# Kernel tuning notes

Hardware: AMD Instinct MI355X
Metric: run time of the kernel (lower is better)

Reference implementation:

```python
import jax, jax.numpy as jnp
import numpy as np

DEPTH = 15  # complete binary tree, N = 2**DEPTH - 1 nodes, heap layout


def setup_inputs() -> dict:
    key = jax.random.key(0)
    ks = jax.random.split(key, 9)
    D, H = 512, 512
    N = 2 ** DEPTH - 1
    s = 0.02
    return {
        "x": jax.random.normal(ks[0], (N, D), jnp.float32),
        "Wi": jax.random.normal(ks[1], (H, D + H), jnp.float32) * s,
        "bi": jax.random.normal(ks[2], (H,), jnp.float32) * s,
        "Wf": jax.random.normal(ks[3], (H, D + H), jnp.float32) * s,
        "bf": jax.random.normal(ks[4], (H,), jnp.float32) * s,
        "Wo": jax.random.normal(ks[5], (H, D + H), jnp.float32) * s,
        "bo": jax.random.normal(ks[6], (H,), jnp.float32) * s,
        "Wu": jax.random.normal(ks[7], (H, D + H), jnp.float32) * s,
        "bu": jax.random.normal(ks[8], (H,), jnp.float32) * s,
    }


def _tree_lstm(x, Wi, bi, Wf, bf, Wo, bo, Wu, bu):
    # Child-Sum Tree-LSTM on a complete binary tree in heap layout.
    # Levels processed bottom-up; each level is fully batched.
    N, D = x.shape
    H = Wi.shape[0]
    sig, tanh = jax.nn.sigmoid, jnp.tanh
    h = jnp.zeros((N, H), x.dtype)
    c = jnp.zeros((N, H), x.dtype)
    for lvl in range(DEPTH - 1, -1, -1):
        start = 2 ** lvl - 1
        cnt = 2 ** lvl
        xl = x[start:start + cnt]  # [cnt, D]
        if lvl == DEPTH - 1:
            # leaf_forward: h_children = 0, no forget gates
            xh = jnp.concatenate([xl, jnp.zeros((cnt, H), x.dtype)], axis=1)
            i = sig(xh @ Wi.T + bi)
            o = sig(xh @ Wo.T + bo)
            u = tanh(xh @ Wu.T + bu)
            cl = i * u
        else:
            cs = 2 * start + 1  # first child index of this level
            ch = h[cs:cs + 2 * cnt].reshape(cnt, 2, H)
            cc = c[cs:cs + 2 * cnt].reshape(cnt, 2, H)
            h_l, h_r = ch[:, 0], ch[:, 1]
            hsum = h_l + h_r  # child-sum
            xh = jnp.concatenate([xl, hsum], axis=1)
            i = sig(xh @ Wi.T + bi)
            o = sig(xh @ Wo.T + bo)
            u = tanh(xh @ Wu.T + bu)
            # per-child forget gates: f_k = sigmoid(Wf @ [x; h_k] + bf)
            f_l = sig(jnp.concatenate([xl, h_l], axis=1) @ Wf.T + bf)
            f_r = sig(jnp.concatenate([xl, h_r], axis=1) @ Wf.T + bf)
            cl = i * u + f_l * cc[:, 0] + f_r * cc[:, 1]
        hl = o * tanh(cl)
        h = h.at[start:start + cnt].set(hl)
        c = c.at[start:start + cnt].set(cl)
    return h[0], c[0]  # root (h, c), matching torch forward's return


def reference(x, Wi, bi, Wf, bf, Wo, bo, Wu, bu):
    return _tree_lstm(x, Wi, bi, Wf, bf, Wo, bo, Wu, bu)
```

## Files before the change

### kernel.cpp

```cpp
#include <hip/hip_runtime.h>

typedef __attribute__((ext_vector_type(8))) short bf16x8;
typedef __attribute__((ext_vector_type(4))) float f32x4;

#define HHE 512

__device__ __forceinline__ unsigned short rne_bf16(float f) {
    union { float f; unsigned u; } v; v.f = f;
    unsigned r = v.u + 0x7FFFu + ((v.u >> 16) & 1u);
    return (unsigned short)(r >> 16);
}
__device__ __forceinline__ float bf2f(unsigned short s) {
    union { unsigned u; float f; } v; v.u = ((unsigned)s) << 16; return v.f;
}
__device__ __forceinline__ float sigf(float v)   { return 1.0f / (1.0f + __expf(-v)); }
__device__ __forceinline__ float tanhf_(float v) { return 2.0f / (1.0f + __expf(-2.0f * v)) - 1.0f; }

#define MFMA16(a, b, c) __builtin_amdgcn_mfma_f32_16x16x32_bf16(a, b, c, 0, 0, 0)

#define GLOAD_LDS16(g, l) \
    __builtin_amdgcn_global_load_lds((const __attribute__((address_space(1))) void*)(g), \
                                     (__attribute__((address_space(3))) void*)(l), 16, 0, 0)

__global__ __launch_bounds__(256) void prep(
    const float* __restrict__ x,
    const float* __restrict__ Wi, const float* __restrict__ Wf,
    const float* __restrict__ Wo, const float* __restrict__ Wu,
    unsigned short* __restrict__ xb, unsigned short* __restrict__ wp,
    int* __restrict__ bar)
{
    const int b = blockIdx.x;
    if (b < 1024) {
        int t    = b * 256 + threadIdx.x;
        if (bar && t == 0) *bar = 0;
        int lane = t & 63;
        int fid  = t >> 6;
        int ks   = fid & 31;
        int jt   = (fid >> 5) & 31;
        int g    = fid >> 10;
        const float* W = (g == 0) ? Wi : (g == 1) ? Wf : (g == 2) ? Wo : Wu;
        int row = jt * 16 + (lane & 15);
        int col = ks * 32 + (lane >> 4) * 8;
        const float* src = W + (size_t)row * 1024 + col;
        float4 f0 = *(const float4*)(src);
        float4 f1 = *(const float4*)(src + 4);
        uint4 o;
        o.x = (unsigned)rne_bf16(f0.x) | ((unsigned)rne_bf16(f0.y) << 16);
        o.y = (unsigned)rne_bf16(f0.z) | ((unsigned)rne_bf16(f0.w) << 16);
        o.z = (unsigned)rne_bf16(f1.x) | ((unsigned)rne_bf16(f1.y) << 16);
        o.w = (unsigned)rne_bf16(f1.z) | ((unsigned)rne_bf16(f1.w) << 16);
        ((uint4*)wp)[t] = o;
    } else {
        size_t idx = (size_t)(b - 1024) * 256 + threadIdx.x;
        if (idx >= 2097088) return;
        const float4* p = (const float4*)x + idx * 2;
        float4 f0 = p[0], f1 = p[1];
        uint4 o;
        o.x = (unsigned)rne_bf16(f0.x) | ((unsigned)rne_bf16(f0.y) << 16);
        o.y = (unsigned)rne_bf16(f0.z) | ((unsigned)rne_bf16(f0.w) << 16);
        o.z = (unsigned)rne_bf16(f1.x) | ((unsigned)rne_bf16(f1.y) << 16);
        o.w = (unsigned)rne_bf16(f1.z) | ((unsigned)rne_bf16(f1.w) << 16);
        ((uint4*)xb)[idx] = o;
    }
}

__global__ __launch_bounds__(256) void leaf_v3(
    const unsigned short* __restrict__ xb, const unsigned short* __restrict__ wp,
    const float* __restrict__ bi, const float* __restrict__ bo, const float* __restrict__ bu,
    unsigned short* __restrict__ hw, unsigned short* __restrict__ cw,
    unsigned short* __restrict__ hso,
    int start, int cnt)
{
    __shared__ __align__(16) unsigned short SH[2 * 2048];

    const int tid  = threadIdx.x;
    const int lane = tid & 63;
    const int wv   = tid >> 6;
    const int q    = lane >> 4;
    const int ln   = lane & 15;
    const int wm   = wv & 1;
    const int wj   = wv >> 1;
    const int mb   = blockIdx.x * 64;
    const int jt0  = blockIdx.y * 4 + wj * 2;

    const int srow   = lane >> 2;
    const int gchunk = (lane & 3) ^ ((lane >> 3) & 3);
    const int stage_row = mb + wv * 16 + srow;
    const int rdoff = ((q ^ ((ln >> 1) & 3)) * 8);

    const unsigned short* wpl = wp + (size_t)lane * 8;

    f32x4 zero = {0.f, 0.f, 0.f, 0.f};
    f32x4 acc_i[2][2], acc_o[2][2], acc_u[2][2];
    #pragma unroll
    for (int t = 0; t < 2; ++t)
        #pragma unroll
        for (int ji = 0; ji < 2; ++ji) {
            acc_i[t][ji] = zero; acc_o[t][ji] = zero; acc_u[t][ji] = zero;
        }

    bf16x8 WA[3][2], WB[3][2];

    auto loadW = [&](bf16x8 (&W)[3][2], int ksabs) {
        #pragma unroll
        for (int g = 0; g < 3; ++g) {
            const int gg = (g == 0) ? 0 : (g + 1);
            #pragma unroll
            for (int ji = 0; ji < 2; ++ji)
                W[g][ji] = *(const bf16x8*)(wpl + ((size_t)((gg * 32 + jt0 + ji) * 32 + ksabs)) * 512);
        }
    };

    loadW(WA, 0);
    {
        const unsigned short* g = xb + (size_t)(start + stage_row) * HHE + gchunk * 8;
        GLOAD_LDS16(g, &SH[0 * 2048 + wv * 512]);
    }
    __syncthreads();

    auto body = [&](int ks, bf16x8 (&WU)[3][2], bf16x8 (&WP)[3][2], int prefks) {
        const int cur = ks & 1;
        if (ks < 15) {
            const unsigned short* g = xb + (size_t)(start + stage_row) * HHE + (ks + 1) * 32 + gchunk * 8;
            GLOAD_LDS16(g, &SH[(cur ^ 1) * 2048 + wv * 512]);
        }
        loadW(WP, prefks);
        bf16x8 a0 = *(const bf16x8*)&SH[cur * 2048 + (wm * 32 + 0 + ln) * 32 + rdoff];
        bf16x8 a1 = *(const bf16x8*)&SH[cur * 2048 + (wm * 32 + 16 + ln) * 32 + rdoff];
        #pragma unroll
        for (int ji = 0; ji < 2; ++ji) {
            acc_i[0][ji] = MFMA16(a0, WU[0][ji], acc_i[0][ji]);
            acc_i[1][ji] = MFMA16(a1, WU[0][ji], acc_i[1][ji]);
            acc_o[0][ji] = MFMA16(a0, WU[1][ji], acc_o[0][ji]);
            acc_o[1][ji] = MFMA16(a1, WU[1][ji], acc_o[1][ji]);
            acc_u[0][ji] = MFMA16(a0, WU[2][ji], acc_u[0][ji]);
            acc_u[1][ji] = MFMA16(a1, WU[2][ji], acc_u[1][ji]);
        }
        __syncthreads();
    };

    for (int kk = 0; kk < 8; ++kk) {
        body(2 * kk,     WA, WB, 2 * kk + 1);
        body(2 * kk + 1, WB, WA, (kk == 7) ? 15 : 2 * kk + 2);
    }

    #pragma unroll
    for (int ji = 0; ji < 2; ++ji) {
        const int jj = (jt0 + ji) * 16 + ln;
        const float bij = bi[jj], boj = bo[jj], buj = bu[jj];
        #pragma unroll
        for (int t = 0; t < 2; ++t) {
            const int n0 = mb + wm * 32 + t * 16 + q * 4;
            float hv[4];
            #pragma unroll
            for (int r = 0; r < 4; ++r) {
                const int node = n0 + r;
                float gi = sigf(acc_i[t][ji][r] + bij);
                float go = sigf(acc_o[t][ji][r] + boj);
                float gu = tanhf_(acc_u[t][ji][r] + buj);
                float cnv = gi * gu;
                float hnv = go * tanhf_(cnv);
                hv[r] = hnv;
                size_t oix = (size_t)node * HHE + jj;
                hw[oix] = rne_bf16(hnv);
                cw[oix] = rne_bf16(cnv);
            }
            hso[(size_t)(n0 >> 1) * HHE + jj]       = rne_bf16(hv[0] + hv[1]);
            hso[(size_t)((n0 >> 1) + 1) * HHE + jj] = rne_bf16(hv[2] + hv[3]);
        }
    }
}

__global__ __launch_bounds__(256) void level_v3(
    const unsigned short* __restrict__ xb, const unsigned short* __restrict__ wp,
    const float* __restrict__ bi, const float* __restrict__ bfv,
    const float* __restrict__ bo, const float* __restrict__ bu,
    const unsigned short* __restrict__ hc, const unsigned short* __restrict__ cc,
    const unsigned short* __restrict__ hs,
    unsigned short* __restrict__ hw, unsigned short* __restrict__ cw,
    unsigned short* __restrict__ hso,
    int start, int cnt)
{
    __shared__ __align__(16) unsigned short SH[2 * 3 * 2048];

    const int tid  = threadIdx.x;
    const int lane = tid & 63;
    const int wv   = tid >> 6;
    const int q    = lane >> 4;
    const int ln   = lane & 15;
    const int wm   = wv & 1;
    const int wj   = wv >> 1;
    const int mb   = blockIdx.x * 64;
    const int jt0  = blockIdx.y * 4 + wj * 2;

    const int srow   = lane >> 2;
    const int gchunk = (lane & 3) ^ ((lane >> 3) & 3);
    const int stage_row = mb + wv * 16 + srow;
    const int rdoff = ((q ^ ((ln >> 1) & 3)) * 8);

    const unsigned short* wpl = wp + (size_t)lane * 8;

    f32x4 zero = {0.f, 0.f, 0.f, 0.f};
    f32x4 acc_i[2][2], acc_f[2][2], acc_o[2][2], acc_u[2][2];
    #pragma unroll
    for (int t = 0; t < 2; ++t)
        #pragma unroll
        for (int ji = 0; ji < 2; ++ji) {
            acc_i[t][ji] = zero; acc_f[t][ji] = zero;
            acc_o[t][ji] = zero; acc_u[t][ji] = zero;
        }

    bf16x8 WA[4][2], WB[4][2];

    auto loadW = [&](bf16x8 (&W)[4][2], int ksabs) {
        #pragma unroll
        for (int g = 0; g < 4; ++g)
            #pragma unroll
            for (int ji = 0; ji < 2; ++ji)
                W[g][ji] = *(const bf16x8*)(wpl + ((size_t)((g * 32 + jt0 + ji) * 32 + ksabs)) * 512);
    };

    loadW(WA, 0);
    {
        const unsigned short* g = xb + (size_t)(start + stage_row) * HHE + gchunk * 8;
        GLOAD_LDS16(g, &SH[(0 * 3 + 0) * 2048 + wv * 512]);
    }
    __syncthreads();

    auto p1_body = [&](int ks, bf16x8 (&WU)[4][2], bf16x8 (&WP)[4][2], int prefks) {
        const int cur = ks & 1;
        if (ks < 15) {
            const unsigned short* g = xb + (size_t)(start + stage_row) * HHE + (ks + 1) * 32 + gchunk * 8;
            GLOAD_LDS16(g, &SH[((cur ^ 1) * 3 + 0) * 2048 + wv * 512]);
        }
        loadW(WP, prefks);
        bf16x8 a0 = *(const bf16x8*)&SH[(cur * 3 + 0) * 2048 + (wm * 32 + 0 + ln) * 32 + rdoff];
        bf16x8 a1 = *(const bf16x8*)&SH[(cur * 3 + 0) * 2048 + (wm * 32 + 16 + ln) * 32 + rdoff];
        #pragma unroll
        for (int ji = 0; ji < 2; ++ji) {
            acc_i[0][ji] = MFMA16(a0, WU[0][ji], acc_i[0][ji]);
            acc_i[1][ji] = MFMA16(a1, WU[0][ji], acc_i[1][ji]);
            acc_f[0][ji] = MFMA16(a0, WU[1][ji], acc_f[0][ji]);
            acc_f[1][ji] = MFMA16(a1, WU[1][ji], acc_f[1][ji]);
            acc_o[0][ji] = MFMA16(a0, WU[2][ji], acc_o[0][ji]);
            acc_o[1][ji] = MFMA16(a1, WU[2][ji], acc_o[1][ji]);
            acc_u[0][ji] = MFMA16(a0, WU[3][ji], acc_u[0][ji]);
            acc_u[1][ji] = MFMA16(a1, WU[3][ji], acc_u[1][ji]);
        }
        __syncthreads();
    };

    for (int kk = 0; kk < 8; ++kk) {
        p1_body(2 * kk,     WA, WB, 2 * kk + 1);
        p1_body(2 * kk + 1, WB, WA, (kk == 7) ? 16 : 2 * kk + 2);
    }

    f32x4 acc_fl[2][2], acc_fr[2][2];
    #pragma unroll
    for (int t = 0; t < 2; ++t)
        #pragma unroll
        for (int ji = 0; ji < 2; ++ji) { acc_fl[t][ji] = acc_f[t][ji]; acc_fr[t][ji] = acc_f[t][ji]; }

    {
        const unsigned short* gs = hs + (size_t)stage_row * HHE + gchunk * 8;
        const unsigned short* gl = hc + ((size_t)(2 * stage_row)) * HHE + gchunk * 8;
        GLOAD_LDS16(gs, &SH[(0 * 3 + 0) * 2048 + wv * 512]);
        GLOAD_LDS16(gl, &SH[(0 * 3 + 1) * 2048 + wv * 512]);
        GLOAD_LDS16(gl + HHE, &SH[(0 * 3 + 2) * 2048 + wv * 512]);
    }
    __syncthreads();

    auto p2_body = [&](int ks, bf16x8 (&WU)[4][2], bf16x8 (&WP)[4][2], int prefks) {
        const int cur = ks & 1;
        if (ks < 15) {
            const unsigned short* gs = hs + (size_t)stage_row * HHE + (ks + 1) * 32 + gchunk * 8;
            const unsigned short* gl = hc + ((size_t)(2 * stage_row)) * HHE + (ks + 1) * 32 + gchunk * 8;
            GLOAD_LDS16(gs, &SH[((cur ^ 1) * 3 + 0) * 2048 + wv * 512]);
            GLOAD_LDS16(gl, &SH[((cur ^ 1) * 3 + 1) * 2048 + wv * 512]);
            GLOAD_LDS16(gl + HHE, &SH[((cur ^ 1) * 3 + 2) * 2048 + wv * 512]);
        }
        loadW(WP, prefks);
        bf16x8 s0 = *(const bf16x8*)&SH[(cur * 3 + 0) * 2048 + (wm * 32 + 0 + ln) * 32 + rdoff];
        bf16x8 s1 = *(const bf16x8*)&SH[(cur * 3 + 0) * 2048 + (wm * 32 + 16 + ln) * 32 + rdoff];
        bf16x8 l0 = *(const bf16x8*)&SH[(cur * 3 + 1) * 2048 + (wm * 32 + 0 + ln) * 32 + rdoff];
        bf16x8 l1 = *(const bf16x8*)&SH[(cur * 3 + 1) * 2048 + (wm * 32 + 16 + ln) * 32 + rdoff];
        bf16x8 r0 = *(const bf16x8*)&SH[(cur * 3 + 2) * 2048 + (wm * 32 + 0 + ln) * 32 + rdoff];
        bf16x8 r1 = *(const bf16x8*)&SH[(cur * 3 + 2) * 2048 + (wm * 32 + 16 + ln) * 32 + rdoff];
        #pragma unroll
        for (int ji = 0; ji < 2; ++ji) {
            acc_i[0][ji]  = MFMA16(s0, WU[0][ji], acc_i[0][ji]);
            acc_i[1][ji]  = MFMA16(s1, WU[0][ji], acc_i[1][ji]);
            acc_o[0][ji]  = MFMA16(s0, WU[2][ji], acc_o[0][ji]);
            acc_o[1][ji]  = MFMA16(s1, WU[2][ji], acc_o[1][ji]);
            acc_u[0][ji]  = MFMA16(s0, WU[3][ji], acc_u[0][ji]);
            acc_u[1][ji]  = MFMA16(s1, WU[3][ji], acc_u[1][ji]);
            acc_fl[0][ji] = MFMA16(l0, WU[1][ji], acc_fl[0][ji]);
            acc_fl[1][ji] = MFMA16(l1, WU[1][ji], acc_fl[1][ji]);
            acc_fr[0][ji] = MFMA16(r0, WU[1][ji], acc_fr[0][ji]);
            acc_fr[1][ji] = MFMA16(r1, WU[1][ji], acc_fr[1][ji]);
        }
        __syncthreads();
    };

    for (int kk = 0; kk < 8; ++kk) {
        p2_body(2 * kk,     WA, WB, 16 + 2 * kk + 1);
        p2_body(2 * kk + 1, WB, WA, (kk == 7) ? 31 : 16 + 2 * kk + 2);
    }

    #pragma unroll
    for (int ji = 0; ji < 2; ++ji) {
        const int jj = (jt0 + ji) * 16 + ln;
        const float bij = bi[jj], bfj = bfv[jj], boj = bo[jj], buj = bu[jj];
        #pragma unroll
        for (int t = 0; t < 2; ++t) {
            const int n0 = mb + wm * 32 + t * 16 + q * 4;
            float hv[4];
            #pragma unroll
            for (int r = 0; r < 4; ++r) {
                const int node = n0 + r;
                size_t cix = (size_t)(2 * node) * HHE + jj;
                float cl = bf2f(cc[cix]);
                float cr = bf2f(cc[cix + HHE]);
                float gi  = sigf(acc_i[t][ji][r] + bij);
                float gfl = sigf(acc_fl[t][ji][r] + bfj);
                float gfr = sigf(acc_fr[t][ji][r] + bfj);
                float go  = sigf(acc_o[t][ji][r] + boj);
                float gu  = tanhf_(acc_u[t][ji][r] + buj);
                float cnv = gi * gu + gfl * cl + gfr * cr;
                float hnv = go * tanhf_(cnv);
                hv[r] = hnv;
                size_t oix = (size_t)node * HHE + jj;
                hw[oix] = rne_bf16(hnv);
                cw[oix] = rne_bf16(cnv);
            }
            hso[(size_t)(n0 >> 1) * HHE + jj]       = rne_bf16(hv[0] + hv[1]);
            hso[(size_t)((n0 >> 1) + 1) * HHE + jj] = rne_bf16(hv[2] + hv[3]);
        }
    }
}

__global__ __launch_bounds__(256) void level_sm(
    const unsigned short* __restrict__ xb, const unsigned short* __restrict__ wp,
    const float* __restrict__ bi, const float* __restrict__ bfv,
    const float* __restrict__ bo, const float* __restrict__ bu,
    const unsigned short* __restrict__ hc, const unsigned short* __restrict__ cc,
    const unsigned short* __restrict__ hs,
    unsigned short* __restrict__ hw, unsigned short* __restrict__ cw,
    unsigned short* __restrict__ hso,
    float* __restrict__ f32out,
    int start, int cnt)
{
    const int tid  = threadIdx.x;
    const int lane = tid & 63;
    const int wv   = tid >> 6;
    const int quad = lane >> 4;
    const int ln   = lane & 15;
    const int mb   = blockIdx.x * 32;
    const int jt   = blockIdx.y * 4 + wv;
    const int j    = jt * 16 + ln;

    int row[2];
    #pragma unroll
    for (int t = 0; t < 2; ++t) {
        int r = mb + t * 16 + ln;
        row[t] = (r < cnt) ? r : (cnt - 1);
    }
    const unsigned short* ax[2];
    #pragma unroll
    for (int t = 0; t < 2; ++t) ax[t] = xb + (size_t)(start + row[t]) * HHE + quad * 8;

    const unsigned short* bw[4];
    #pragma unroll
    for (int g = 0; g < 4; ++g) bw[g] = wp + ((size_t)(g * 32 + jt) * 32) * 512 + lane * 8;

    f32x4 zero = {0.f, 0.f, 0.f, 0.f};
    f32x4 acc_i[2], acc_f[2], acc_o[2], acc_u[2];
    #pragma unroll
    for (int t = 0; t < 2; ++t) { acc_i[t] = zero; acc_f[t] = zero; acc_o[t] = zero; acc_u[t] = zero; }

    #pragma unroll 4
    for (int ks = 0; ks < 16; ++ks) {
        bf16x8 a[2];
        #pragma unroll
        for (int t = 0; t < 2; ++t) { a[t] = *(const bf16x8*)ax[t]; ax[t] += 32; }
        bf16x8 b0 = *(const bf16x8*)bw[0]; bw[0] += 512;
        bf16x8 b1 = *(const bf16x8*)bw[1]; bw[1] += 512;
        bf16x8 b2 = *(const bf16x8*)bw[2]; bw[2] += 512;
        bf16x8 b3 = *(const bf16x8*)bw[3]; bw[3] += 512;
        #pragma unroll
        for (int t = 0; t < 2; ++t) {
            acc_i[t] = MFMA16(a[t], b0, acc_i[t]);
            acc_f[t] = MFMA16(a[t], b1, acc_f[t]);
            acc_o[t] = MFMA16(a[t], b2, acc_o[t]);
            acc_u[t] = MFMA16(a[t], b3, acc_u[t]);
        }
    }

    f32x4 acc_fl[2], acc_fr[2];
    #pragma unroll
    for (int t = 0; t < 2; ++t) { acc_fl[t] = acc_f[t]; acc_fr[t] = acc_f[t]; }

    const unsigned short* as[2];
    const unsigned short* al[2];
    const unsigned short* ar[2];
    #pragma unroll
    for (int t = 0; t < 2; ++t) {
        as[t] = hs + (size_t)row[t] * HHE + quad * 8;
        al[t] = hc + (size_t)(2 * row[t]) * HHE + quad * 8;
        ar[t] = al[t] + HHE;
    }

    #pragma unroll 4
    for (int ks = 0; ks < 16; ++ks) {
        bf16x8 b0 = *(const bf16x8*)bw[0]; bw[0] += 512;
        bf16x8 b1 = *(const bf16x8*)bw[1]; bw[1] += 512;
        bf16x8 b2 = *(const bf16x8*)bw[2]; bw[2] += 512;
        bf16x8 b3 = *(const bf16x8*)bw[3]; bw[3] += 512;
        bf16x8 s[2];
        #pragma unroll
        for (int t = 0; t < 2; ++t) { s[t] = *(const bf16x8*)as[t]; as[t] += 32; }
        #pragma unroll
        for (int t = 0; t < 2; ++t) {
            acc_i[t] = MFMA16(s[t], b0, acc_i[t]);
            acc_o[t] = MFMA16(s[t], b2, acc_o[t]);
            acc_u[t] = MFMA16(s[t], b3, acc_u[t]);
        }
        bf16x8 l[2];
        #pragma unroll
        for (int t = 0; t < 2; ++t) { l[t] = *(const bf16x8*)al[t]; al[t] += 32; }
        #pragma unroll
        for (int t = 0; t < 2; ++t) acc_fl[t] = MFMA16(l[t], b1, acc_fl[t]);
        bf16x8 rr[2];
        #pragma unroll
        for (int t = 0; t < 2; ++t) { rr[t] = *(const bf16x8*)ar[t]; ar[t] += 32; }
        #pragma unroll
        for (int t = 0; t < 2; ++t) acc_fr[t] = MFMA16(rr[t], b1, acc_fr[t]);
    }

    const float bij = bi[j], bfj = bfv[j], boj = bo[j], buj = bu[j];
    #pragma unroll
    for (int t = 0; t < 2; ++t) {
        const int n0 = mb + t * 16 + quad * 4;
        float hv[4];
        #pragma unroll
        for (int r = 0; r < 4; ++r) {
            const int node = n0 + r;
            const int ncl  = (node < cnt) ? node : (cnt - 1);
            size_t cix = (size_t)(2 * ncl) * HHE + j;
            float cl = bf2f(cc[cix]);
            float cr = bf2f(cc[cix + HHE]);
            float gi  = sigf(acc_i[t][r] + bij);
            float gfl = sigf(acc_fl[t][r] + bfj);
            float gfr = sigf(acc_fr[t][r] + bfj);
            float go  = sigf(acc_o[t][r] + boj);
            float gu  = tanhf_(acc_u[t][r] + buj);
            float cnv = gi * gu + gfl * cl + gfr * cr;
            float hnv = go * tanhf_(cnv);
            hv[r] = hnv;
            if (node < cnt) {
                size_t oix = (size_t)node * HHE + j;
                hw[oix] = rne_bf16(hnv);
                cw[oix] = rne_bf16(cnv);
                if (f32out) {
                    f32out[(size_t)node * 1024 + j]       = hnv;
                    f32out[(size_t)node * 1024 + 512 + j] = cnv;
                }
            }
        }
        if (n0 + 1 < cnt) hso[(size_t)(n0 >> 1) * HHE + j]       = rne_bf16(hv[0] + hv[1]);
        if (n0 + 3 < cnt) hso[(size_t)((n0 >> 1) + 1) * HHE + j] = rne_bf16(hv[2] + hv[3]);
    }
}

#define TAIL_NBLK 32

__device__ __forceinline__ void tailbar(int* bar, int target) {
    __syncthreads();
    if (threadIdx.x == 0) {
        __threadfence();
        __hip_atomic_fetch_add(bar, 1, __ATOMIC_RELAXED, __HIP_MEMORY_SCOPE_AGENT);
        while (__hip_atomic_load(bar, __ATOMIC_RELAXED, __HIP_MEMORY_SCOPE_AGENT) < target)
            __builtin_amdgcn_s_sleep(2);
        __threadfence();
    }
    __syncthreads();
}

__global__ __launch_bounds__(256) void tail_fused(
    const unsigned short* __restrict__ xb, const unsigned short* __restrict__ wp,
    const float* __restrict__ bi, const float* __restrict__ bfv,
    const float* __restrict__ bo, const float* __restrict__ bu,
    unsigned short* __restrict__ hA, unsigned short* __restrict__ cA,
    unsigned short* __restrict__ hB, unsigned short* __restrict__ cB,
    unsigned short* __restrict__ hs1, unsigned short* __restrict__ hs2,
    float* __restrict__ out, int* __restrict__ bar)
{
    __shared__ __align__(16) unsigned short WL[128 * 512];

    const int tid  = threadIdx.x;
    const int lane = tid & 63;
    const int wv   = tid >> 6;
    const int quad = lane >> 4;
    const int ln   = lane & 15;
    const int jt   = blockIdx.x;
    const int j    = jt * 16 + ln;
    const int wl   = lane * 8;

    #pragma unroll
    for (int i = 0; i < 32; ++i) {
        int f = i * 4 + wv;
        const unsigned short* src = wp + ((size_t)(((f >> 5) * 32 + jt) * 32 + (f & 31))) * 512 + lane * 8;
        GLOAD_LDS16(src, &WL[f * 512]);
    }
    __syncthreads();

    const float bij = bi[j], bfj = bfv[j], boj = bo[j], buj = bu[j];

    int k = 0;
    for (int lvl = 6; lvl >= 0; --lvl) {
        const int cnt = 1 << lvl;
        const int start = cnt - 1;
        const unsigned short *hc, *cc, *hs;
        unsigned short *hw, *cw, *hso;
        if (lvl & 1) { hc = hA; cc = cA; hs = hs1; hw = hB; cw = cB; hso = hs2; }
        else         { hc = hB; cc = cB; hs = hs2; hw = hA; cw = cA; hso = hs1; }

        const int r0  = wv * 16 + ln;
        const int row = (r0 < cnt) ? r0 : (cnt - 1);

        f32x4 zero = {0.f, 0.f, 0.f, 0.f};
        f32x4 acc_i = zero, acc_f = zero, acc_o = zero, acc_u = zero;

        const unsigned short* ax = xb + (size_t)(start + row) * HHE + quad * 8;
        #pragma unroll 4
        for (int ks = 0; ks < 16; ++ks) {
            bf16x8 a  = *(const bf16x8*)ax; ax += 32;
            bf16x8 w0 = *(const bf16x8*)&WL[(0 * 32 + ks) * 512 + wl];
            bf16x8 w1 = *(const bf16x8*)&WL[(1 * 32 + ks) * 512 + wl];
            bf16x8 w2 = *(const bf16x8*)&WL[(2 * 32 + ks) * 512 + wl];
            bf16x8 w3 = *(const bf16x8*)&WL[(3 * 32 + ks) * 512 + wl];
            acc_i = MFMA16(a, w0, acc_i);
            acc_f = MFMA16(a, w1, acc_f);
            acc_o = MFMA16(a, w2, acc_o);
            acc_u = MFMA16(a, w3, acc_u);
        }

        f32x4 acc_fl = acc_f, acc_fr = acc_f;
        const unsigned short* as = hs + (size_t)row * HHE + quad * 8;
        const unsigned short* al = hc + (size_t)(2 * row) * HHE + quad * 8;
        const unsigned short* ar = al + HHE;
        #pragma unroll 4
        for (int ks = 0; ks < 16; ++ks) {
            bf16x8 w0 = *(const bf16x8*)&WL[(0 * 32 + 16 + ks) * 512 + wl];
            bf16x8 w1 = *(const bf16x8*)&WL[(1 * 32 + 16 + ks) * 512 + wl];
            bf16x8 w2 = *(const bf16x8*)&WL[(2 * 32 + 16 + ks) * 512 + wl];
            bf16x8 w3 = *(const bf16x8*)&WL[(3 * 32 + 16 + ks) * 512 + wl];
            bf16x8 s  = *(const bf16x8*)as; as += 32;
            bf16x8 l  = *(const bf16x8*)al; al += 32;
            bf16x8 rr = *(const bf16x8*)ar; ar += 32;
            acc_i  = MFMA16(s,  w0, acc_i);
            acc_o  = MFMA16(s,  w2, acc_o);
            acc_u  = MFMA16(s,  w3, acc_u);
            acc_fl = MFMA16(l,  w1, acc_fl);
            acc_fr = MFMA16(rr, w1, acc_fr);
        }

        const int n0 = wv * 16 + quad * 4;
        float hv[4];
        #pragma unroll
        for (int r = 0; r < 4; ++r) {
            const int node = n0 + r;
            const int ncl  = (node < cnt) ? node : (cnt - 1);
            size_t cix = (size_t)(2 * ncl) * HHE + j;
            float cl = bf2f(cc[cix]);
            float cr = bf2f(cc[cix + HHE]);
            float gi  = sigf(acc_i[r] + bij);
            float gfl = sigf(acc_fl[r] + bfj);
            float gfr = sigf(acc_fr[r] + bfj);
            float go  = sigf(acc_o[r] + boj);
            float gu  = tanhf_(acc_u[r] + buj);
            float cnv = gi * gu + gfl * cl + gfr * cr;
            float hnv = go * tanhf_(cnv);
            hv[r] = hnv;
            if (node < cnt) {
                size_t oix = (size_t)node * HHE + j;
                hw[oix] = rne_bf16(hnv);
                cw[oix] = rne_bf16(cnv);
                if (lvl == 0) {
                    out[(size_t)node * 1024 + j]       = hnv;
                    out[(size_t)node * 1024 + 512 + j] = cnv;
                }
            }
        }
        if (n0 + 1 < cnt) hso[(size_t)(n0 >> 1) * HHE + j]       = rne_bf16(hv[0] + hv[1]);
        if (n0 + 3 < cnt) hso[(size_t)((n0 >> 1) + 1) * HHE + j] = rne_bf16(hv[2] + hv[3]);

        if (lvl > 0) { ++k; tailbar(bar, TAIL_NBLK * k); }
    }
}

extern "C" void kernel_launch(void* const* d_in, const int* in_sizes, int n_in,
                              void* d_out, int out_size, void* d_ws, size_t ws_size,
                              hipStream_t stream) {
    const float* x  = (const float*)d_in[0];
    const float* Wi = (const float*)d_in[1];
    const float* bi = (const float*)d_in[2];
    const float* Wf = (const float*)d_in[3];
    const float* bf = (const float*)d_in[4];
    const float* Wo = (const float*)d_in[5];
    const float* bo = (const float*)d_in[6];
    const float* Wu = (const float*)d_in[7];
    const float* bu = (const float*)d_in[8];
    float* out = (float*)d_out;

    unsigned short* xb  = (unsigned short*)d_ws;
    unsigned short* wp  = xb  + 16776704;
    unsigned short* hA  = wp  + 2097152;
    unsigned short* hB  = hA  + 8388608;
    unsigned short* hs1 = hB  + 4194304;
    unsigned short* hs2 = hs1 + 4194304;
    unsigned short* cA  = hs2 + 2097152;
    unsigned short* cB  = cA  + 8388608;

    const size_t BAR_OFF = (size_t)96 << 20;
    const bool fused = ws_size >= BAR_OFF + 64;
    int* bar = (int*)((char*)d_ws + BAR_OFF);

    prep<<<9216, 256, 0, stream>>>(x, Wi, Wf, Wo, Wu, xb, wp, fused ? bar : nullptr);

    leaf_v3<<<dim3(256, 8), 256, 0, stream>>>(xb, wp, bi, bo, bu, hA, cA, hs1, 16383, 16384);

    for (int lvl = 13; lvl >= 7; --lvl) {
        int cnt   = 1 << lvl;
        int start = cnt - 1;
        const unsigned short *hc, *cc, *hs;
        unsigned short *hw, *cw, *hso;
        if (lvl & 1) { hc = hA; cc = cA; hs = hs1; hw = hB; cw = cB; hso = hs2; }
        else         { hc = hB; cc = cB; hs = hs2; hw = hA; cw = cA; hso = hs1; }
        level_v3<<<dim3(cnt / 64, 8), 256, 0, stream>>>(xb, wp, bi, bf, bo, bu,
                                                        hc, cc, hs, hw, cw, hso, start, cnt);
    }

    if (fused) {
        tail_fused<<<TAIL_NBLK, 256, 0, stream>>>(xb, wp, bi, bf, bo, bu,
                                                  hA, cA, hB, cB, hs1, hs2, out, bar);
    } else {
        level_v3<<<dim3(1, 8), 256, 0, stream>>>(xb, wp, bi, bf, bo, bu,
                                                 hB, cB, hs2, hA, cA, hs1, 63, 64);
        for (int lvl = 5; lvl >= 0; --lvl) {
            int cnt   = 1 << lvl;
            int start = cnt - 1;
            const unsigned short *hc, *cc, *hs;
            unsigned short *hw, *cw, *hso;
            if (lvl & 1) { hc = hA; cc = cA; hs = hs1; hw = hB; cw = cB; hso = hs2; }
            else         { hc = hB; cc = cB; hs = hs2; hw = hA; cw = cA; hso = hs1; }
            float* f32out = (lvl == 0) ? out : nullptr;
            level_sm<<<dim3((cnt + 31) / 32, 8), 256, 0, stream>>>(xb, wp, bi, bf, bo, bu,
                                                                   hc, cc, hs, hw, cw, hso, f32out,
                                                                   start, cnt);
        }
    }
}
```

Before: 517.8 us.

## Overlap next-level x-projection with grid barrier wait in tail kernel

Splits the tail level loop so the x-part of the gate GEMM for the next level (independent of child states) is computed between arriving at and waiting on the inter-block barrier. This hides barrier latency behind MFMA work. The h/c stores become relaxed agent-scope atomic stores, and the explicit threadfences are replaced by an acquire fence after the barrier. That drops the full release fence before the arrive, which risks memory-ordering correctness if the relaxed stores and increment are not ordered.

```diff
diff --git a/kernel.cpp b/kernel.cpp
--- a/kernel.cpp
+++ b/kernel.cpp
@@ -21,6 +21,8 @@
 #define GLOAD_LDS16(g, l) \
     __builtin_amdgcn_global_load_lds((const __attribute__((address_space(1))) void*)(g), \
                                      (__attribute__((address_space(3))) void*)(l), 16, 0, 0)
+
+#define CSTORE_US(p, v) __hip_atomic_store((p), (v), __ATOMIC_RELAXED, __HIP_MEMORY_SCOPE_AGENT)
 
 __global__ __launch_bounds__(256) void prep(
     const float* __restrict__ x,
@@ -474,18 +476,6 @@
 
 #define TAIL_NBLK 32
 
-__device__ __forceinline__ void tailbar(int* bar, int target) {
-    __syncthreads();
-    if (threadIdx.x == 0) {
-        __threadfence();
-        __hip_atomic_fetch_add(bar, 1, __ATOMIC_RELAXED, __HIP_MEMORY_SCOPE_AGENT);
-        while (__hip_atomic_load(bar, __ATOMIC_RELAXED, __HIP_MEMORY_SCOPE_AGENT) < target)
-            __builtin_amdgcn_s_sleep(2);
-        __threadfence();
-    }
-    __syncthreads();
-}
-
 __global__ __launch_bounds__(256) void tail_fused(
     const unsigned short* __restrict__ xb, const unsigned short* __restrict__ wp,
     const float* __restrict__ bi, const float* __restrict__ bfv,
@@ -515,22 +505,14 @@
     __syncthreads();
 
     const float bij = bi[j], bfj = bfv[j], boj = bo[j], buj = bu[j];
-
-    int k = 0;
-    for (int lvl = 6; lvl >= 0; --lvl) {
+    f32x4 zero = {0.f, 0.f, 0.f, 0.f};
+
+    auto phase1 = [&](int lvl, f32x4& pi, f32x4& pf, f32x4& po, f32x4& pu) {
         const int cnt = 1 << lvl;
         const int start = cnt - 1;
-        const unsigned short *hc, *cc, *hs;
-        unsigned short *hw, *cw, *hso;
-        if (lvl & 1) { hc = hA; cc = cA; hs = hs1; hw = hB; cw = cB; hso = hs2; }
-        else         { hc = hB; cc = cB; hs = hs2; hw = hA; cw = cA; hso = hs1; }
-
         const int r0  = wv * 16 + ln;
         const int row = (r0 < cnt) ? r0 : (cnt - 1);
-
-        f32x4 zero = {0.f, 0.f, 0.f, 0.f};
-        f32x4 acc_i = zero, acc_f = zero, acc_o = zero, acc_u = zero;
-
+        pi = zero; pf = zero; po = zero; pu = zero;
         const unsigned short* ax = xb + (size_t)(start + row) * HHE + quad * 8;
         #pragma unroll 4
         for (int ks = 0; ks < 16; ++ks) {
@@ -539,13 +521,30 @@
             bf16x8 w1 = *(const bf16x8*)&WL[(1 * 32 + ks) * 512 + wl];
             bf16x8 w2 = *(const bf16x8*)&WL[(2 * 32 + ks) * 512 + wl];
             bf16x8 w3 = *(const bf16x8*)&WL[(3 * 32 + ks) * 512 + wl];
-            acc_i = MFMA16(a, w0, acc_i);
-            acc_f = MFMA16(a, w1, acc_f);
-            acc_o = MFMA16(a, w2, acc_o);
-            acc_u = MFMA16(a, w3, acc_u);
-        }
-
-        f32x4 acc_fl = acc_f, acc_fr = acc_f;
+            pi = MFMA16(a, w0, pi);
+            pf = MFMA16(a, w1, pf);
+            po = MFMA16(a, w2, po);
+            pu = MFMA16(a, w3, pu);
+        }
+    };
+
+    f32x4 p_i, p_f, p_o, p_u;
+    phase1(6, p_i, p_f, p_o, p_u);
+
+    int k = 0;
+    for (int lvl = 6; lvl >= 0; --lvl) {
+        const int cnt = 1 << lvl;
+        const unsigned short *hc, *cc, *hs;
+        unsigned short *hw, *cw, *hso;
+        if (lvl & 1) { hc = hA; cc = cA; hs = hs1; hw = hB; cw = cB; hso = hs2; }
+        else         { hc = hB; cc = cB; hs = hs2; hw = hA; cw = cA; hso = hs1; }
+
+        const int r0  = wv * 16 + ln;
+        const int row = (r0 < cnt) ? r0 : (cnt - 1);
+
+        f32x4 acc_i = p_i, acc_o = p_o, acc_u = p_u;
+        f32x4 acc_fl = p_f, acc_fr = p_f;
+
         const unsigned short* as = hs + (size_t)row * HHE + quad * 8;
         const unsigned short* al = hc + (size_t)(2 * row) * HHE + quad * 8;
         const unsigned short* ar = al + HHE;
@@ -584,18 +583,30 @@
             hv[r] = hnv;
             if (node < cnt) {
                 size_t oix = (size_t)node * HHE + j;
-                hw[oix] = rne_bf16(hnv);
-                cw[oix] = rne_bf16(cnv);
+                CSTORE_US(&hw[oix], rne_bf16(hnv));
+                CSTORE_US(&cw[oix], rne_bf16(cnv));
                 if (lvl == 0) {
                     out[(size_t)node * 1024 + j]       = hnv;
                     out[(size_t)node * 1024 + 512 + j] = cnv;
                 }
             }
         }
-        if (n0 + 1 < cnt) hso[(size_t)(n0 >> 1) * HHE + j]       = rne_bf16(hv[0] + hv[1]);
-        if (n0 + 3 < cnt) hso[(size_t)((n0 >> 1) + 1) * HHE + j] = rne_bf16(hv[2] + hv[3]);
-
-        if (lvl > 0) { ++k; tailbar(bar, TAIL_NBLK * k); }
+        if (n0 + 1 < cnt) CSTORE_US(&hso[(size_t)(n0 >> 1) * HHE + j],       rne_bf16(hv[0] + hv[1]));
+        if (n0 + 3 < cnt) CSTORE_US(&hso[(size_t)((n0 >> 1) + 1) * HHE + j], rne_bf16(hv[2] + hv[3]));
+
+        if (lvl > 0) {
+            ++k;
+            __syncthreads();
+            if (tid == 0)
+                __hip_atomic_fetch_add(bar, 1, __ATOMIC_RELAXED, __HIP_MEMORY_SCOPE_AGENT);
+            phase1(lvl - 1, p_i, p_f, p_o, p_u);
+            if (tid == 0) {
+                while (__hip_atomic_load(bar, __ATOMIC_RELAXED, __HIP_MEMORY_SCOPE_AGENT) < TAIL_NBLK * k)
+                    __builtin_amdgcn_s_sleep(2);
+            }
+            __syncthreads();
+            __builtin_amdgcn_fence(__ATOMIC_ACQUIRE, "agent");
+        }
     }
 }
 
```

Measured after the change: 511.2 us. About the same (-1.3%).
